# Optimization experiments

Measured on AMD Instinct MI355X. Metric: run time of the kernel, lower is better.

## Reference

```python
import jax, jax.numpy as jnp
import numpy as np

B, Q, C, N, H, W = 2, 4096, 256, 6, 64, 96
HEADS, POINTS = 8, 4


def _grid_sample(img, grid):
    # img: [G, C, H, W]; grid: [G, P, 2] in [-1,1]
    # bilinear, align_corners=False, padding_mode='zeros' (matches F.grid_sample)
    G, Cc, Hh, Ww = img.shape
    gx = (grid[..., 0] + 1.0) * (Ww / 2.0) - 0.5
    gy = (grid[..., 1] + 1.0) * (Hh / 2.0) - 0.5
    x0f = jnp.floor(gx)
    y0f = jnp.floor(gy)
    wx = (gx - x0f)[:, None, :]
    wy = (gy - y0f)[:, None, :]
    x0 = x0f.astype(jnp.int32)
    y0 = y0f.astype(jnp.int32)
    flat = img.reshape(G, Cc, Hh * Ww)

    def gather(xi, yi):
        valid = ((xi >= 0) & (xi < Ww) & (yi >= 0) & (yi < Hh))
        idx = jnp.clip(yi, 0, Hh - 1) * Ww + jnp.clip(xi, 0, Ww - 1)
        v = jnp.take_along_axis(flat, idx[:, None, :], axis=2)  # [G,C,P]
        return v * valid[:, None, :].astype(img.dtype)

    v00 = gather(x0, y0)
    v01 = gather(x0 + 1, y0)
    v10 = gather(x0, y0 + 1)
    v11 = gather(x0 + 1, y0 + 1)
    return (v00 * (1 - wx) * (1 - wy) + v01 * wx * (1 - wy)
            + v10 * (1 - wx) * wy + v11 * wx * wy)


def setup_inputs() -> dict:
    key = jax.random.key(0)
    ks = jax.random.split(key, 12)
    query = jax.random.normal(ks[0], (B, Q, C), dtype=jnp.float32)
    query_coords = jax.random.uniform(ks[1], (B, Q, 3), dtype=jnp.float32)
    image_feats = jax.random.normal(ks[2], (B, N, C, H, W), dtype=jnp.float32)
    # realistic f-theta fisheye intrinsics for 1280x1080 images
    Kmat = np.array([[500.0, 0.0, 640.0], [0.0, 500.0, 540.0], [0.0, 0.0, 1.0]], dtype=np.float32)
    intrinsics = jnp.asarray(np.tile(Kmat, (B, N, 1, 1)))
    # inverse extrinsics: identity rotation, cameras 3m behind the voxel volume (cam_z > 0)
    E = np.tile(np.eye(4, dtype=np.float32), (B, N, 1, 1))
    for n in range(N):
        E[:, n, 0, 3] = 0.2 * n - 0.5
        E[:, n, 2, 3] = 3.0
    inv_extrinsics = jnp.asarray(E)
    s = 1.0 / np.sqrt(C)
    W_off = jax.random.normal(ks[3], (C, N * HEADS * POINTS * 2), dtype=jnp.float32) * 0.02
    b_off = jnp.zeros((N * HEADS * POINTS * 2,), dtype=jnp.float32)
    W_attn = jax.random.normal(ks[4], (C, N * HEADS * POINTS), dtype=jnp.float32) * s
    b_attn = jnp.zeros((N * HEADS * POINTS,), dtype=jnp.float32)
    W_val = jax.random.normal(ks[5], (C, C), dtype=jnp.float32) * s
    b_val = jax.random.normal(ks[6], (C,), dtype=jnp.float32) * 0.01
    W_out = jax.random.normal(ks[7], (C, C), dtype=jnp.float32) * s
    b_out = jax.random.normal(ks[8], (C,), dtype=jnp.float32) * 0.01
    return {"query": query, "query_coords": query_coords, "image_feats": image_feats,
            "intrinsics": intrinsics, "inv_extrinsics": inv_extrinsics,
            "W_off": W_off, "b_off": b_off, "W_attn": W_attn, "b_attn": b_attn,
            "W_val": W_val, "b_val": b_val, "W_out": W_out, "b_out": b_out}


def reference(query, query_coords, image_feats, intrinsics, inv_extrinsics,
              W_off, b_off, W_attn, b_attn, W_val, b_val, W_out, b_out):
    Bq, Qq, Cq = query.shape
    _, Nn, _, Hh, Ww = image_feats.shape
    hd = Cq // HEADS
    # ---- reference points: voxel coords -> world -> camera -> f-theta image ----
    xmin, ymin, zmin, xmax, ymax, zmax = -3.6, -3.0, -0.7, 3.6, 3.0, 2.5
    rx = query_coords[..., 0] * (xmax - xmin) + xmin
    ry = query_coords[..., 1] * (ymax - ymin) + ymin
    rz = query_coords[..., 2] * (zmax - zmin) + zmin
    world = jnp.stack([rx, ry, rz, jnp.ones_like(rx)], axis=-1)  # [B,Q,4]
    cam = jnp.einsum('bnij,bqj->bnqi', inv_extrinsics, world)    # [B,N,Q,4]
    cxp, cyp, czp = cam[..., 0], cam[..., 1], cam[..., 2]
    r3d = jnp.sqrt(cxp * cxp + cyp * cyp + 1e-8)
    theta = jnp.arctan2(r3d, czp)
    phi = jnp.arctan2(cyp, cxp)
    fx = intrinsics[:, :, 0, 0][..., None]
    cx0 = intrinsics[:, :, 0, 2][..., None]
    cy0 = intrinsics[:, :, 1, 2][..., None]
    r_img = fx * theta
    u = r_img * jnp.cos(phi) + cx0
    v = r_img * jnp.sin(phi) + cy0
    origH, origW = 1080, 1280
    ref = jnp.stack([2.0 * u / (origW - 1) - 1.0, 2.0 * v / (origH - 1) - 1.0], axis=-1)  # [B,N,Q,2]
    fov = ((czp > 0) & (theta < 1.372)).astype(query.dtype)      # [B,N,Q]
    # ---- offsets + attention weights ----
    offs = jnp.tanh((query @ W_off + b_off).reshape(Bq, Qq, Nn, HEADS, POINTS, 2)) * 0.5
    aw = (query @ W_attn + b_attn).reshape(Bq, Qq, Nn, HEADS, POINTS)
    aw = aw * jnp.transpose(fov, (0, 2, 1))[..., None, None]
    aw = jax.nn.softmax(aw, axis=-1)
    # ---- value projection ----
    val = jnp.einsum('bnchw,cd->bnhwd', image_feats, W_val) + b_val  # [B,N,H,W,C]
    val = val.reshape(Bq, Nn, Hh, Ww, HEADS, hd)
    # ---- sampling locations ----
    locs = ref[:, :, :, None, None, :] + jnp.transpose(offs, (0, 2, 1, 3, 4, 5))  # [B,N,Q,h,p,2]
    v_all = jnp.transpose(val, (0, 1, 4, 5, 2, 3)).reshape(Bq * Nn * HEADS, hd, Hh, Ww)
    locs_all = jnp.transpose(locs, (0, 1, 3, 2, 4, 5)).reshape(Bq * Nn * HEADS, Qq * POINTS, 2)
    sampled = _grid_sample(v_all, locs_all).reshape(Bq, Nn, HEADS, hd, Qq, POINTS)
    sampled = jnp.transpose(sampled, (0, 4, 1, 2, 5, 3))  # [B,Q,N,heads,points,hd]
    weighted = jnp.sum(sampled * aw[..., None], axis=4)   # [B,Q,N,heads,hd]
    out = weighted.sum(axis=2).reshape(Bq, Qq, Cq)
    return out @ W_out + b_out
```

## Files before the change

kernel.cpp:

```cpp
#include <hip/hip_runtime.h>
#include <math.h>

#define Bb 2
#define Qq 4096
#define Cc 256
#define Nn 6
#define Hh 64
#define Ww 96
#define HEADS 8
#define POINTS 4
#define HW (Hh*Ww)
#define BQ (Bb*Qq)

#define WS_VAL   0
#define WS_WTF   9437184
#define WS_WCHF  9469952
#define WS_WCLF  9543680
#define WS_WOTF  9617408
#define WS_LOCS  18874368
#define WS_AW    22020096
#define WS_REFF  23592960
#define WS_WSUM  23740416

typedef __attribute__((ext_vector_type(8))) short short8;
typedef __attribute__((ext_vector_type(4))) float f32x4;

__device__ __forceinline__ unsigned short f2bf(float f) {
    union { float f; unsigned u; } v; v.f = f;
    unsigned r = (v.u + 0x7fffu + ((v.u >> 16) & 1u)) >> 16;
    return (unsigned short)r;
}
__device__ __forceinline__ float bf2f(unsigned short h) { return __uint_as_float((unsigned)h << 16); }
__device__ __forceinline__ float bflo(unsigned u) { return __uint_as_float(u << 16); }
__device__ __forceinline__ float bfhi(unsigned u) { return __uint_as_float(u & 0xffff0000u); }
__device__ __forceinline__ unsigned packbf(float a, float b) {
    return (unsigned)f2bf(a) | ((unsigned)f2bf(b) << 16);
}

__global__ void prep_kernel(const float* __restrict__ qc,
                            const float* __restrict__ intr,
                            const float* __restrict__ invE,
                            float* __restrict__ reff,
                            const float* __restrict__ Wv,
                            const float* __restrict__ Wo,
                            const float* __restrict__ Wa,
                            const float* __restrict__ Wu,
                            unsigned short* __restrict__ Wtf,
                            unsigned short* __restrict__ Wchf,
                            unsigned short* __restrict__ Wclf,
                            unsigned short* __restrict__ Wotf) {
    int blk = blockIdx.x;
    int tid = threadIdx.x;
    if (blk < 32) {
        int idx = blk * 256 + tid;
        int b = idx >> 12;
        int q = idx & (Qq - 1);
        float rx = qc[idx*3+0] * 7.2f - 3.6f;
        float ry = qc[idx*3+1] * 6.0f - 3.0f;
        float rz = qc[idx*3+2] * 3.2f - 0.7f;
        for (int n = 0; n < Nn; ++n) {
            const float* E = invE + (b*Nn+n)*16;
            float camx = E[0]*rx + E[1]*ry + E[2]*rz  + E[3];
            float camy = E[4]*rx + E[5]*ry + E[6]*rz  + E[7];
            float camz = E[8]*rx + E[9]*ry + E[10]*rz + E[11];
            const float* K = intr + (b*Nn+n)*9;
            float fx = K[0], cx0 = K[2], cy0 = K[5];
            float r3d   = sqrtf(camx*camx + camy*camy + 1e-8f);
            float theta = atan2f(r3d, camz);
            float phi   = atan2f(camy, camx);
            float r_img = fx * theta;
            float u = r_img * cosf(phi) + cx0;
            float v = r_img * sinf(phi) + cy0;
            int base = ((b*Nn+n)*Qq + q)*3;
            reff[base+0] = 2.0f * u / 1279.0f - 1.0f;
            reff[base+1] = 2.0f * v / 1079.0f - 1.0f;
            reff[base+2] = (camz > 0.0f && theta < 1.372f) ? 1.0f : 0.0f;
        }
        return;
    }
    int idx = (blk - 32) * 256 + tid;
    if (idx < 65536) {
        int s = idx & 7, l = (idx >> 3) & 63, kk = (idx >> 9) & 7, t = idx >> 12;
        int n = t*16 + (l & 15);
        int k = kk*32 + (l >> 4)*8 + s;
        Wtf[idx] = f2bf(Wv[k*256 + n]);
    } else if (idx < 212992) {
        int i2 = idx - 65536;
        int s = i2 & 7, l = (i2 >> 3) & 63, kk = (i2 >> 9) & 7, t = i2 >> 12;
        int n = t*16 + (l & 15);
        int k = kk*32 + (l >> 4)*8 + s;
        float w = (n < 384) ? Wo[k*384 + n] : Wa[k*192 + (n - 384)];
        unsigned short h = f2bf(w);
        Wchf[i2] = h;
        Wclf[i2] = f2bf(w - bf2f(h));
    } else {
        int i3 = idx - 212992;
        int s = i3 & 7, l = (i3 >> 3) & 63, kk = (i3 >> 9) & 7, t = i3 >> 12;
        int n = t*16 + (l & 15);
        int k = kk*32 + (l >> 4)*8 + s;
        Wotf[i3] = f2bf(Wu[k*256 + n]);
    }
}

__global__ __launch_bounds__(512, 2) void vp_mfma_kernel(const float* __restrict__ feats,
                                                         const unsigned short* __restrict__ Wtf,
                                                         const float* __restrict__ bv,
                                                         unsigned short* __restrict__ val) {
    __shared__ __align__(16) unsigned short As[64 * 272];
    int t = threadIdx.x;
    int pix0 = blockIdx.x * 64;
    int bn = blockIdx.y;
    const float* A = feats + (size_t)bn * Cc * HW + pix0;
    int lane = t & 63, wavei = t >> 6, quad = lane >> 4, l15 = lane & 15;
    {
        int pq = t & 15;
        int oct = t >> 4;
        float va[8][4];
#pragma unroll
        for (int j = 0; j < 8; ++j)
            *(float4*)va[j] = *(const float4*)&A[(size_t)(oct*8 + j)*HW + pq*4];
#pragma unroll
        for (int e = 0; e < 4; ++e) {
            int m = pq*4 + e;
            uint4 pk;
            pk.x = packbf(va[0][e], va[1][e]);
            pk.y = packbf(va[2][e], va[3][e]);
            pk.z = packbf(va[4][e], va[5][e]);
            pk.w = packbf(va[6][e], va[7][e]);
            *(uint4*)&As[m*264 + oct*8] = pk;
        }
    }
    __syncthreads();
    int wm = wavei & 1;
    int wn = wavei >> 1;
    int r0 = wm*32 + l15, r1 = r0 + 16;
    const unsigned short* Wl = Wtf + (size_t)lane * 8;
#define VP_BOFF(nt, kk) ((size_t)(((wn*4 + (nt))*8 + (kk)) << 9))
    f32x4 acc[2][4];
#pragma unroll
    for (int i = 0; i < 2; ++i)
#pragma unroll
        for (int j = 0; j < 4; ++j) acc[i][j] = (f32x4){0.f, 0.f, 0.f, 0.f};
    short8 bA[4], bB[4];
#pragma unroll
    for (int nt = 0; nt < 4; ++nt) bA[nt] = *(const short8*)&Wl[VP_BOFF(nt, 0)];
#pragma unroll
    for (int kk = 0; kk < 8; kk += 2) {
        if (kk + 1 < 8) {
#pragma unroll
            for (int nt = 0; nt < 4; ++nt) bB[nt] = *(const short8*)&Wl[VP_BOFF(nt, kk+1)];
        }
        {
            short8 a0 = *(const short8*)&As[r0*264 + kk*32 + quad*8];
            short8 a1 = *(const short8*)&As[r1*264 + kk*32 + quad*8];
#pragma unroll
            for (int nt = 0; nt < 4; ++nt) {
                acc[0][nt] = __builtin_amdgcn_mfma_f32_16x16x32_bf16(a0, bA[nt], acc[0][nt], 0, 0, 0);
                acc[1][nt] = __builtin_amdgcn_mfma_f32_16x16x32_bf16(a1, bA[nt], acc[1][nt], 0, 0, 0);
            }
        }
        if (kk + 2 < 8) {
#pragma unroll
            for (int nt = 0; nt < 4; ++nt) bA[nt] = *(const short8*)&Wl[VP_BOFF(nt, kk+2)];
        }
        if (kk + 1 < 8) {
            int k1 = kk + 1;
            short8 a0 = *(const short8*)&As[r0*264 + k1*32 + quad*8];
            short8 a1 = *(const short8*)&As[r1*264 + k1*32 + quad*8];
#pragma unroll
            for (int nt = 0; nt < 4; ++nt) {
                acc[0][nt] = __builtin_amdgcn_mfma_f32_16x16x32_bf16(a0, bB[nt], acc[0][nt], 0, 0, 0);
                acc[1][nt] = __builtin_amdgcn_mfma_f32_16x16x32_bf16(a1, bB[nt], acc[1][nt], 0, 0, 0);
            }
        }
    }
    __syncthreads();
#pragma unroll
    for (int nt = 0; nt < 4; ++nt) {
        int n = wn*64 + nt*16 + l15;
        float bias = bv[n];
#pragma unroll
        for (int mt = 0; mt < 2; ++mt) {
#pragma unroll
            for (int r = 0; r < 4; ++r) {
                int mm = wm*32 + mt*16 + quad*4 + r;
                As[mm*272 + n] = f2bf(acc[mt][nt][r] + bias);
            }
        }
    }
    __syncthreads();
#pragma unroll
    for (int i = 0; i < 4; ++i) {
        int flat = wavei*2048 + i*512 + lane*8;
        int pix = flat >> 8, ch = flat & 255;
        int head = ch >> 5, c32 = ch & 31;
        *(uint4*)&val[(((size_t)bn*HEADS + head)*HW + pix0 + pix)*32 + c32] =
            *(const uint4*)&As[pix*272 + ch];
    }
}

__global__ __launch_bounds__(512, 2) void qp_kernel(const float* __restrict__ query,
                                                    const unsigned short* __restrict__ Wchf,
                                                    const unsigned short* __restrict__ Wclf,
                                                    const float* __restrict__ b_off,
                                                    const float* __restrict__ b_attn,
                                                    const float* __restrict__ reff,
                                                    float* __restrict__ locs,
                                                    float* __restrict__ aw) {
    __shared__ __align__(16) unsigned short Ah[32 * 256];
    __shared__ __align__(16) unsigned short Al[32 * 256];
    int t = threadIdx.x;
    int row0 = blockIdx.x * 32;
    {
        int row = t & 31;
        int c2 = t >> 5;
        const float* src = query + (size_t)(row0 + row) * 256;
#pragma unroll
        for (int cc = 0; cc < 2; ++cc) {
            int c = c2 * 2 + cc;
            float4 v0 = *(const float4*)&src[c*8 + 0];
            float4 v1 = *(const float4*)&src[c*8 + 4];
            float f[8] = {v0.x, v0.y, v0.z, v0.w, v1.x, v1.y, v1.z, v1.w};
            unsigned short h[8], l[8];
#pragma unroll
            for (int j = 0; j < 8; ++j) {
                h[j] = f2bf(f[j]);
                l[j] = f2bf(f[j] - bf2f(h[j]));
            }
            uint4 ph, pl;
            ph.x = h[0] | ((unsigned)h[1] << 16); ph.y = h[2] | ((unsigned)h[3] << 16);
            ph.z = h[4] | ((unsigned)h[5] << 16); ph.w = h[6] | ((unsigned)h[7] << 16);
            pl.x = l[0] | ((unsigned)l[1] << 16); pl.y = l[2] | ((unsigned)l[3] << 16);
            pl.z = l[4] | ((unsigned)l[5] << 16); pl.w = l[6] | ((unsigned)l[7] << 16);
            int pos = row * 256 + ((c ^ row) << 3);
            *(uint4*)&Ah[pos] = ph;
            *(uint4*)&Al[pos] = pl;
        }
    }
    __syncthreads();
    int wave = t >> 6, lane = t & 63, quad = lane >> 4, l15 = lane & 15;
    int ms = wave & 1;
    int ng = wave >> 1;
    int arow = ms*16 + l15;
    int bq = row0 >> 12;
#pragma unroll
    for (int ib = 0; ib < 3; ++ib) {
        f32x4 acc[3];
#pragma unroll
        for (int i = 0; i < 3; ++i) acc[i] = (f32x4){0.f, 0.f, 0.f, 0.f};
        int col0 = ng*144 + ib*48;
        int tile0 = ng*9 + ib*3;
#pragma unroll
        for (int kk = 0; kk < 8; ++kk) {
            int apos = arow*256 + (((kk*4+quad) ^ arow) << 3);
            short8 a_h = *(const short8*)&Ah[apos];
            short8 a_l = *(const short8*)&Al[apos];
#pragma unroll
            for (int i = 0; i < 3; ++i) {
                bool prec = (col0 + i*16) < 384;
                size_t fb = ((size_t)((tile0 + i)*8 + kk) << 9) + lane*8;
                short8 b_h = *(const short8*)&Wchf[fb];
                acc[i] = __builtin_amdgcn_mfma_f32_16x16x32_bf16(a_h, b_h, acc[i], 0, 0, 0);
                if (prec) {
                    short8 b_l = *(const short8*)&Wclf[fb];
                    acc[i] = __builtin_amdgcn_mfma_f32_16x16x32_bf16(a_l, b_h, acc[i], 0, 0, 0);
                    acc[i] = __builtin_amdgcn_mfma_f32_16x16x32_bf16(a_h, b_l, acc[i], 0, 0, 0);
                }
            }
        }
#pragma unroll
        for (int i = 0; i < 3; ++i) {
            int tcol = col0 + i*16;
            int j = tcol + l15;
            if (tcol < 384) {
                int n_cam = j >> 6;
                int xy = j & 1;
                float bias = b_off[j];
#pragma unroll
                for (int r = 0; r < 4; ++r) {
                    int q = row0 + ms*16 + quad*4 + r;
                    int qq = q & (Qq-1);
                    float refv = reff[((bq*Nn + n_cam)*Qq + qq)*3 + xy];
                    locs[(size_t)q*384 + j] = refv + tanhf(acc[i][r] + bias) * 0.5f;
                }
            } else {
                int j2 = j - 384;
                int n_cam = j2 >> 5;
                float bias = b_attn[j2];
#pragma unroll
                for (int r = 0; r < 4; ++r) {
                    int q = row0 + ms*16 + quad*4 + r;
                    int qq = q & (Qq-1);
                    float fov = reff[((bq*Nn + n_cam)*Qq + qq)*3 + 2];
                    float lg = (acc[i][r] + bias) * fov;
                    float mx = fmaxf(lg, __shfl_xor(lg, 1));
                    mx = fmaxf(mx, __shfl_xor(mx, 2));
                    float e = expf(lg - mx);
                    float s = e + __shfl_xor(e, 1);
                    s = s + __shfl_xor(s, 2);
                    aw[(size_t)q*192 + j2] = e / s;
                }
            }
        }
    }
}

__global__ __launch_bounds__(256, 4) void samp_kernel(const unsigned short* __restrict__ val,
                                                      const float* __restrict__ locs,
                                                      const float* __restrict__ aw,
                                                      unsigned short* __restrict__ wsum) {
    __shared__ float swgt[4][4][200];
    __shared__ int   soff[4][4][200];
    int t = threadIdx.x, wv = t >> 6, lane = t & 63;
    int q = blockIdx.x * 4 + wv;
    int b = q >> 12;
#pragma unroll
    for (int j = 0; j < 3; ++j) {
        int s = lane + 64*j;
        float2 xy = *(const float2*)&locs[(size_t)q*384 + 2*s];
        float w = aw[(size_t)q*192 + s];
        float gx = (xy.x + 1.0f)*48.0f - 0.5f;
        float gy = (xy.y + 1.0f)*32.0f - 0.5f;
        float x0f = floorf(gx), y0f = floorf(gy);
        float wx = gx - x0f, wy = gy - y0f;
        int ix = (int)x0f, iy = (int)y0f;
        bool vx0 = (unsigned)ix       < (unsigned)Ww;
        bool vx1 = (unsigned)(ix + 1) < (unsigned)Ww;
        bool vy0 = (unsigned)iy       < (unsigned)Hh;
        bool vy1 = (unsigned)(iy + 1) < (unsigned)Hh;
        int ix0 = min(max(ix, 0), Ww-1), ix1 = min(max(ix+1, 0), Ww-1);
        int iy0 = min(max(iy, 0), Hh-1), iy1 = min(max(iy+1, 0), Hh-1);
        swgt[wv][0][s] = (vx0 && vy0) ? w*(1.0f-wx)*(1.0f-wy) : 0.0f;
        swgt[wv][1][s] = (vx1 && vy0) ? w*wx*(1.0f-wy)        : 0.0f;
        swgt[wv][2][s] = (vx0 && vy1) ? w*(1.0f-wx)*wy        : 0.0f;
        swgt[wv][3][s] = (vx1 && vy1) ? w*wx*wy               : 0.0f;
        soff[wv][0][s] = (iy0*Ww + ix0) * 64;
        soff[wv][1][s] = (iy0*Ww + ix1) * 64;
        soff[wv][2][s] = (iy1*Ww + ix0) * 64;
        soff[wv][3][s] = (iy1*Ww + ix1) * 64;
    }
    __syncthreads();
    int cg   = lane >> 5;
    int head = (lane >> 2) & 7;
    int oc   = lane & 3;
    const char* vbase = (const char*)val + (size_t)(b*Nn*HEADS + head)*HW*64 + oc*16;
    float a[8] = {0.f,0.f,0.f,0.f,0.f,0.f,0.f,0.f};
#pragma unroll
    for (int n = 0; n < Nn; ++n) {
        const char* vb = vbase + (size_t)n*HEADS*HW*64;
#pragma unroll
        for (int p = 0; p < POINTS; ++p) {
            int s = (n*HEADS + head)*POINTS + p;
            float w0 = swgt[wv][cg*2+0][s];
            float w1 = swgt[wv][cg*2+1][s];
            int   o0 = soff[wv][cg*2+0][s];
            int   o1 = soff[wv][cg*2+1][s];
            uint4 u0 = *(const uint4*)(vb + o0);
            uint4 u1 = *(const uint4*)(vb + o1);
            a[0] += w0*bflo(u0.x); a[1] += w0*bfhi(u0.x);
            a[2] += w0*bflo(u0.y); a[3] += w0*bfhi(u0.y);
            a[4] += w0*bflo(u0.z); a[5] += w0*bfhi(u0.z);
            a[6] += w0*bflo(u0.w); a[7] += w0*bfhi(u0.w);
            a[0] += w1*bflo(u1.x); a[1] += w1*bfhi(u1.x);
            a[2] += w1*bflo(u1.y); a[3] += w1*bfhi(u1.y);
            a[4] += w1*bflo(u1.z); a[5] += w1*bfhi(u1.z);
            a[6] += w1*bflo(u1.w); a[7] += w1*bfhi(u1.w);
        }
    }
#pragma unroll
    for (int j = 0; j < 8; ++j) a[j] += __shfl_xor(a[j], 32);
    if (cg == 0) {
        int c = head*32 + oc*8;
        uint4 o;
        o.x = packbf(a[0], a[1]);
        o.y = packbf(a[2], a[3]);
        o.z = packbf(a[4], a[5]);
        o.w = packbf(a[6], a[7]);
        *(uint4*)&wsum[(size_t)q*256 + c] = o;
    }
}

__global__ __launch_bounds__(256) void out_mfma_kernel(const unsigned short* __restrict__ wsum,
                                                       const unsigned short* __restrict__ Wotf,
                                                       const float* __restrict__ b_out,
                                                       float* __restrict__ out) {
    int t = threadIdx.x;
    int row0 = blockIdx.x * 64;
    int col0 = blockIdx.y * 128;
    int wave = t >> 6, lane = t & 63, quad = lane >> 4, l15 = lane & 15;
    int wm = wave & 1;
    int wn = wave >> 1;
    f32x4 acc[2][4];
#pragma unroll
    for (int i = 0; i < 2; ++i)
#pragma unroll
        for (int j = 0; j < 4; ++j) acc[i][j] = (f32x4){0.f, 0.f, 0.f, 0.f};
#pragma unroll
    for (int kk = 0; kk < 8; ++kk) {
        short8 a[2];
#pragma unroll
        for (int mt = 0; mt < 2; ++mt)
            a[mt] = *(const short8*)&wsum[(size_t)(row0 + wm*32 + mt*16 + l15)*256 + kk*32 + quad*8];
#pragma unroll
        for (int nt = 0; nt < 4; ++nt) {
            size_t fb = ((size_t)((blockIdx.y*8 + wn*4 + nt)*8 + kk) << 9) + lane*8;
            short8 bfr = *(const short8*)&Wotf[fb];
            acc[0][nt] = __builtin_amdgcn_mfma_f32_16x16x32_bf16(a[0], bfr, acc[0][nt], 0, 0, 0);
            acc[1][nt] = __builtin_amdgcn_mfma_f32_16x16x32_bf16(a[1], bfr, acc[1][nt], 0, 0, 0);
        }
    }
#pragma unroll
    for (int nt = 0; nt < 4; ++nt) {
        int col = col0 + wn*64 + nt*16 + l15;
        float bias = b_out[col];
#pragma unroll
        for (int mt = 0; mt < 2; ++mt) {
#pragma unroll
            for (int r = 0; r < 4; ++r) {
                int q = row0 + wm*32 + mt*16 + quad*4 + r;
                out[(size_t)q*256 + col] = acc[mt][nt][r] + bias;
            }
        }
    }
}

extern "C" void kernel_launch(void* const* d_in, const int* in_sizes, int n_in,
                              void* d_out, int out_size, void* d_ws, size_t ws_size,
                              hipStream_t stream) {
    const float* query  = (const float*)d_in[0];
    const float* qc     = (const float*)d_in[1];
    const float* feats  = (const float*)d_in[2];
    const float* intr   = (const float*)d_in[3];
    const float* invE   = (const float*)d_in[4];
    const float* W_off  = (const float*)d_in[5];
    const float* b_off  = (const float*)d_in[6];
    const float* W_attn = (const float*)d_in[7];
    const float* b_attn = (const float*)d_in[8];
    const float* W_val  = (const float*)d_in[9];
    const float* b_val  = (const float*)d_in[10];
    const float* W_out  = (const float*)d_in[11];
    const float* b_out  = (const float*)d_in[12];
    float* out = (float*)d_out;
    float* ws  = (float*)d_ws;
    unsigned short* val  = (unsigned short*)(ws + WS_VAL);
    unsigned short* Wtf  = (unsigned short*)(ws + WS_WTF);
    unsigned short* Wchf = (unsigned short*)(ws + WS_WCHF);
    unsigned short* Wclf = (unsigned short*)(ws + WS_WCLF);
    unsigned short* Wotf = (unsigned short*)(ws + WS_WOTF);
    float* locs = ws + WS_LOCS;
    float* aw   = ws + WS_AW;
    float* reff = ws + WS_REFF;
    unsigned short* wsum = (unsigned short*)(ws + WS_WSUM);

    hipLaunchKernelGGL(prep_kernel, dim3(1120), dim3(256), 0, stream,
                       qc, intr, invE, reff, W_val, W_off, W_attn, W_out,
                       Wtf, Wchf, Wclf, Wotf);
    hipLaunchKernelGGL(vp_mfma_kernel, dim3(HW/64, Bb*Nn), dim3(512), 0, stream,
                       feats, Wtf, b_val, val);
    hipLaunchKernelGGL(qp_kernel, dim3(BQ/32), dim3(512), 0, stream,
                       query, Wchf, Wclf, b_off, b_attn, reff, locs, aw);
    hipLaunchKernelGGL(samp_kernel, dim3(BQ/4), dim3(256), 0, stream,
                       val, locs, aw, wsum);
    hipLaunchKernelGGL(out_mfma_kernel, dim3(BQ/64, 2), dim3(256), 0, stream,
                       wsum, Wotf, b_out, out);
}
```

Measured before the change: 265.0 us.

## Split qp_kernel columns across grid y and double-buffer weight loads

The query-projection kernel now runs as a 3-wide grid in y. Two slices compute the 384 offset columns using split-precision (3 MFMAs), and the third computes the 192 attention columns using single bf16 MFMAs. Each wave handles only 3 tiles instead of 9, its B-fragment global loads are software-pipelined with ping-pong registers, and launch bounds are raised to 4 blocks per CU. This adds parallelism and hides load latency, but each y-slice repeats the query load and bf16 split into LDS, tripling that work.

```diff
diff --git a/kernel.cpp b/kernel.cpp
--- a/kernel.cpp
+++ b/kernel.cpp
@@ -199,7 +199,7 @@
     }
 }
 
-__global__ __launch_bounds__(512, 2) void qp_kernel(const float* __restrict__ query,
+__global__ __launch_bounds__(512, 4) void qp_kernel(const float* __restrict__ query,
                                                     const unsigned short* __restrict__ Wchf,
                                                     const unsigned short* __restrict__ Wclf,
                                                     const float* __restrict__ b_off,
@@ -211,6 +211,7 @@
     __shared__ __align__(16) unsigned short Al[32 * 256];
     int t = threadIdx.x;
     int row0 = blockIdx.x * 32;
+    int ty = blockIdx.y;
     {
         int row = t & 31;
         int c2 = t >> 5;
@@ -243,66 +244,125 @@
     int ng = wave >> 1;
     int arow = ms*16 + l15;
     int bq = row0 >> 12;
-#pragma unroll
-    for (int ib = 0; ib < 3; ++ib) {
-        f32x4 acc[3];
-#pragma unroll
-        for (int i = 0; i < 3; ++i) acc[i] = (f32x4){0.f, 0.f, 0.f, 0.f};
-        int col0 = ng*144 + ib*48;
-        int tile0 = ng*9 + ib*3;
-#pragma unroll
-        for (int kk = 0; kk < 8; ++kk) {
-            int apos = arow*256 + (((kk*4+quad) ^ arow) << 3);
-            short8 a_h = *(const short8*)&Ah[apos];
-            short8 a_l = *(const short8*)&Al[apos];
-#pragma unroll
-            for (int i = 0; i < 3; ++i) {
-                bool prec = (col0 + i*16) < 384;
-                size_t fb = ((size_t)((tile0 + i)*8 + kk) << 9) + lane*8;
-                short8 b_h = *(const short8*)&Wchf[fb];
-                acc[i] = __builtin_amdgcn_mfma_f32_16x16x32_bf16(a_h, b_h, acc[i], 0, 0, 0);
-                if (prec) {
-                    short8 b_l = *(const short8*)&Wclf[fb];
-                    acc[i] = __builtin_amdgcn_mfma_f32_16x16x32_bf16(a_l, b_h, acc[i], 0, 0, 0);
-                    acc[i] = __builtin_amdgcn_mfma_f32_16x16x32_bf16(a_h, b_l, acc[i], 0, 0, 0);
+    int tile0 = ty*12 + ng*3;
+    f32x4 acc[3];
+#pragma unroll
+    for (int i = 0; i < 3; ++i) acc[i] = (f32x4){0.f, 0.f, 0.f, 0.f};
+
+#define QP_FB(i, kk) (((size_t)((tile0 + (i))*8 + (kk)) << 9) + lane*8)
+
+    if (ty < 2) {
+        short8 bhA[3], blA[3], bhB[3], blB[3];
+#pragma unroll
+        for (int i = 0; i < 3; ++i) {
+            bhA[i] = *(const short8*)&Wchf[QP_FB(i, 0)];
+            blA[i] = *(const short8*)&Wclf[QP_FB(i, 0)];
+        }
+#pragma unroll
+        for (int kk = 0; kk < 8; kk += 2) {
+            if (kk + 1 < 8) {
+#pragma unroll
+                for (int i = 0; i < 3; ++i) {
+                    bhB[i] = *(const short8*)&Wchf[QP_FB(i, kk+1)];
+                    blB[i] = *(const short8*)&Wclf[QP_FB(i, kk+1)];
                 }
             }
+            {
+                int apos = arow*256 + (((kk*4+quad) ^ arow) << 3);
+                short8 a_h = *(const short8*)&Ah[apos];
+                short8 a_l = *(const short8*)&Al[apos];
+#pragma unroll
+                for (int i = 0; i < 3; ++i) {
+                    acc[i] = __builtin_amdgcn_mfma_f32_16x16x32_bf16(a_h, bhA[i], acc[i], 0, 0, 0);
+                    acc[i] = __builtin_amdgcn_mfma_f32_16x16x32_bf16(a_l, bhA[i], acc[i], 0, 0, 0);
+                    acc[i] = __builtin_amdgcn_mfma_f32_16x16x32_bf16(a_h, blA[i], acc[i], 0, 0, 0);
+                }
+            }
+            if (kk + 2 < 8) {
+#pragma unroll
+                for (int i = 0; i < 3; ++i) {
+                    bhA[i] = *(const short8*)&Wchf[QP_FB(i, kk+2)];
+                    blA[i] = *(const short8*)&Wclf[QP_FB(i, kk+2)];
+                }
+            }
+            if (kk + 1 < 8) {
+                int k1 = kk + 1;
+                int apos = arow*256 + (((k1*4+quad) ^ arow) << 3);
+                short8 a_h = *(const short8*)&Ah[apos];
+                short8 a_l = *(const short8*)&Al[apos];
+#pragma unroll
+                for (int i = 0; i < 3; ++i) {
+                    acc[i] = __builtin_amdgcn_mfma_f32_16x16x32_bf16(a_h, bhB[i], acc[i], 0, 0, 0);
+                    acc[i] = __builtin_amdgcn_mfma_f32_16x16x32_bf16(a_l, bhB[i], acc[i], 0, 0, 0);
+                    acc[i] = __builtin_amdgcn_mfma_f32_16x16x32_bf16(a_h, blB[i], acc[i], 0, 0, 0);
+                }
+            }
         }
 #pragma unroll
         for (int i = 0; i < 3; ++i) {
-            int tcol = col0 + i*16;
-            int j = tcol + l15;
-            if (tcol < 384) {
-                int n_cam = j >> 6;
-                int xy = j & 1;
-                float bias = b_off[j];
-#pragma unroll
-                for (int r = 0; r < 4; ++r) {
-                    int q = row0 + ms*16 + quad*4 + r;
-                    int qq = q & (Qq-1);
-                    float refv = reff[((bq*Nn + n_cam)*Qq + qq)*3 + xy];
-                    locs[(size_t)q*384 + j] = refv + tanhf(acc[i][r] + bias) * 0.5f;
-                }
-            } else {
-                int j2 = j - 384;
-                int n_cam = j2 >> 5;
-                float bias = b_attn[j2];
-#pragma unroll
-                for (int r = 0; r < 4; ++r) {
-                    int q = row0 + ms*16 + quad*4 + r;
-                    int qq = q & (Qq-1);
-                    float fov = reff[((bq*Nn + n_cam)*Qq + qq)*3 + 2];
-                    float lg = (acc[i][r] + bias) * fov;
-                    float mx = fmaxf(lg, __shfl_xor(lg, 1));
-                    mx = fmaxf(mx, __shfl_xor(mx, 2));
-                    float e = expf(lg - mx);
-                    float s = e + __shfl_xor(e, 1);
-                    s = s + __shfl_xor(s, 2);
-                    aw[(size_t)q*192 + j2] = e / s;
-                }
-            }
-        }
-    }
+            int j = (tile0 + i)*16 + l15;
+            int n_cam = j >> 6;
+            int xy = j & 1;
+            float bias = b_off[j];
+#pragma unroll
+            for (int r = 0; r < 4; ++r) {
+                int q = row0 + ms*16 + quad*4 + r;
+                int qq = q & (Qq-1);
+                float refv = reff[((bq*Nn + n_cam)*Qq + qq)*3 + xy];
+                locs[(size_t)q*384 + j] = refv + tanhf(acc[i][r] + bias) * 0.5f;
+            }
+        }
+    } else {
+        short8 bhA[3], bhB[3];
+#pragma unroll
+        for (int i = 0; i < 3; ++i) bhA[i] = *(const short8*)&Wchf[QP_FB(i, 0)];
+#pragma unroll
+        for (int kk = 0; kk < 8; kk += 2) {
+            if (kk + 1 < 8) {
+#pragma unroll
+                for (int i = 0; i < 3; ++i) bhB[i] = *(const short8*)&Wchf[QP_FB(i, kk+1)];
+            }
+            {
+                int apos = arow*256 + (((kk*4+quad) ^ arow) << 3);
+                short8 a_h = *(const short8*)&Ah[apos];
+#pragma unroll
+                for (int i = 0; i < 3; ++i)
+                    acc[i] = __builtin_amdgcn_mfma_f32_16x16x32_bf16(a_h, bhA[i], acc[i], 0, 0, 0);
+            }
+            if (kk + 2 < 8) {
+#pragma unroll
+                for (int i = 0; i < 3; ++i) bhA[i] = *(const short8*)&Wchf[QP_FB(i, kk+2)];
+            }
+            if (kk + 1 < 8) {
+                int k1 = kk + 1;
+                int apos = arow*256 + (((k1*4+quad) ^ arow) << 3);
+                short8 a_h = *(const short8*)&Ah[apos];
+#pragma unroll
+                for (int i = 0; i < 3; ++i)
+                    acc[i] = __builtin_amdgcn_mfma_f32_16x16x32_bf16(a_h, bhB[i], acc[i], 0, 0, 0);
+            }
+        }
+#pragma unroll
+        for (int i = 0; i < 3; ++i) {
+            int j2 = (tile0 + i)*16 + l15 - 384;
+            int n_cam = j2 >> 5;
+            float bias = b_attn[j2];
+#pragma unroll
+            for (int r = 0; r < 4; ++r) {
+                int q = row0 + ms*16 + quad*4 + r;
+                int qq = q & (Qq-1);
+                float fov = reff[((bq*Nn + n_cam)*Qq + qq)*3 + 2];
+                float lg = (acc[i][r] + bias) * fov;
+                float mx = fmaxf(lg, __shfl_xor(lg, 1));
+                mx = fmaxf(mx, __shfl_xor(mx, 2));
+                float e = expf(lg - mx);
+                float s = e + __shfl_xor(e, 1);
+                s = s + __shfl_xor(s, 2);
+                aw[(size_t)q*192 + j2] = e / s;
+            }
+        }
+    }
+#undef QP_FB
 }
 
 __global__ __launch_bounds__(256, 4) void samp_kernel(const unsigned short* __restrict__ val,
@@ -457,7 +517,7 @@
                        Wtf, Wchf, Wclf, Wotf);
     hipLaunchKernelGGL(vp_mfma_kernel, dim3(HW/64, Bb*Nn), dim3(512), 0, stream,
                        feats, Wtf, b_val, val);
-    hipLaunchKernelGGL(qp_kernel, dim3(BQ/32), dim3(512), 0, stream,
+    hipLaunchKernelGGL(qp_kernel, dim3(BQ/32, 3), dim3(512), 0, stream,
                        query, Wchf, Wclf, b_off, b_attn, reff, locs, aw);
     hipLaunchKernelGGL(samp_kernel, dim3(BQ/4), dim3(256), 0, stream,
                        val, locs, aw, wsum);
```

After: 237.2 us. -10.5%, faster.
